# Optimization experiments

Hardware: AMD Instinct MI355X
Metric: run time of the kernel (lower is better)

## Reference

```python
import jax, jax.numpy as jnp
import numpy as np

EPS = 1e-5  # torch BatchNorm2d default eps


def setup_inputs() -> dict:
    key = jax.random.key(0)
    ks = jax.random.split(key, 11)
    n, c, h, w = 16, 512, 64, 64
    grp, cg, mip = 4, 128, 16
    return {
        "x": jax.random.normal(ks[0], (n, c, h, w), dtype=jnp.float32),
        "W1": jax.random.normal(ks[1], (mip, cg), dtype=jnp.float32) * 0.05,
        "b1": jax.random.normal(ks[2], (mip,), dtype=jnp.float32) * 0.05,
        "gamma": jax.random.uniform(ks[3], (mip,), dtype=jnp.float32, minval=0.5, maxval=1.5),
        "beta": jax.random.normal(ks[4], (mip,), dtype=jnp.float32) * 0.05,
        "mean": jax.random.normal(ks[5], (mip,), dtype=jnp.float32) * 0.05,
        "var": jax.random.uniform(ks[6], (mip,), dtype=jnp.float32, minval=0.5, maxval=1.5),
        "Wh": jax.random.normal(ks[7], (cg, mip), dtype=jnp.float32) * 0.1,
        "bh": jax.random.normal(ks[8], (cg,), dtype=jnp.float32) * 0.05,
        "Ww": jax.random.normal(ks[9], (cg, mip), dtype=jnp.float32) * 0.1,
        "bw": jax.random.normal(ks[10], (cg,), dtype=jnp.float32) * 0.05,
    }


def reference(x, W1, b1, gamma, beta, mean, var, Wh, bh, Ww, bw):
    n, c, h, w = x.shape
    grp = 4
    cg = c // grp
    # Since c % 4 == 0, torch.split gives 4 equal groups: fold group into a new axis.
    xg = x.reshape(n, grp, cg, h, w)                       # (n,g,cg,h,w)
    gh = xg.mean(axis=4)                                   # pool over w -> (n,g,cg,h)
    gw = xg.mean(axis=3)                                   # pool over h -> (n,g,cg,w)
    y = jnp.concatenate([gh, gw], axis=3)                  # (n,g,cg,h+w)
    # conv1 (1x1) shared across all 4 groups
    y = jnp.einsum('ngcl,mc->ngml', y, W1) + b1[None, None, :, None]
    # BatchNorm2d (eval mode, running stats)
    scale = gamma / jnp.sqrt(var + EPS)
    y = y * scale[None, None, :, None] + (beta - mean * scale)[None, None, :, None]
    # h_swish: x * relu6(x+3)/6
    y = y * (jnp.clip(y + 3.0, 0.0, 6.0) / 6.0)
    yh, yw = y[..., :h], y[..., h:]                        # (n,g,mip,h), (n,g,mip,w)
    a_h = jax.nn.sigmoid(jnp.einsum('ngml,cm->ngcl', yh, Wh) + bh[None, None, :, None])
    a_w = jax.nn.sigmoid(jnp.einsum('ngml,cm->ngcl', yw, Ww) + bw[None, None, :, None])
    out = xg * a_h[..., :, None] * a_w[..., None, :]       # (n,g,cg,h,w)
    out = out.reshape(n, c, h, w)
    # channel shuffle: (n, cg, grp, h, w) -> permute group axis forward
    out = out.reshape(n, cg, grp, h, w).transpose(0, 2, 1, 3, 4).reshape(n, c, h, w)
    return out
```

## Files before the change

kernel.cpp:

```cpp
#include <hip/hip_runtime.h>

#define N_   16
#define C_   512
#define GRP  4
#define CG   128
#define MIP  16

__device__ __forceinline__ float bf_lo(unsigned u) { return __uint_as_float(u << 16); }
__device__ __forceinline__ float bf_hi(unsigned u) { return __uint_as_float(u & 0xFFFF0000u); }
__device__ __forceinline__ float bf1(unsigned short s) { return __uint_as_float((unsigned)s << 16); }

__device__ __forceinline__ float ld_scalar(const void* p, int i, bool isbf) {
    return isbf ? bf1(((const unsigned short*)p)[i]) : ((const float*)p)[i];
}

__device__ __forceinline__ bool sniff_isbf(const unsigned* __restrict__ x32,
                                           int t, unsigned* s_flag) {
    if (t < 64) {
        int cnt = 0;
        #pragma unroll
        for (int k = 0; k < 4; ++k) {
            unsigned w = x32[t + 64 * k];
            unsigned e = (w >> 7) & 0xFFu;
            cnt += (e >= 0x60u && e <= 0x9Fu) ? 1 : 0;
        }
        #pragma unroll
        for (int off = 32; off > 0; off >>= 1) cnt += __shfl_down(cnt, off, 64);
        if (t == 0) *s_flag = (cnt >= 192) ? 1u : 0u;
    }
    __syncthreads();
    return *s_flag != 0u;
}

__global__ __launch_bounds__(256) void kreduce(const void* __restrict__ xv,
                                               float* __restrict__ gh,
                                               float* __restrict__ gw) {
    __shared__ float scratch[32][65];
    __shared__ unsigned flag_s;
    const int bid = blockIdx.x;
    const int t = threadIdx.x;
    const bool isbf = sniff_isbf((const unsigned*)xv, t, &flag_s);

    if (isbf) {
        const uint4* src = (const uint4*)((const unsigned short*)xv + (size_t)bid * 4096);
        float cp[8] = {0,0,0,0,0,0,0,0};
        #pragma unroll
        for (int hf = 0; hf < 2; ++hf) {
            int idx = t + hf * 256;
            int r = idx >> 3;
            uint4 v = src[idx];
            unsigned uu[4] = {v.x, v.y, v.z, v.w};
            float rp = 0.f;
            #pragma unroll
            for (int k = 0; k < 4; ++k) {
                float f0 = bf_lo(uu[k]), f1 = bf_hi(uu[k]);
                rp += f0 + f1;
                cp[2*k] += f0; cp[2*k+1] += f1;
            }
            rp += __shfl_xor(rp, 1);
            rp += __shfl_xor(rp, 2);
            rp += __shfl_xor(rp, 4);
            if ((t & 7) == 0) gh[(size_t)bid * 64 + r] = rp * (1.f/64.f);
        }
        #pragma unroll
        for (int k = 0; k < 8; ++k) scratch[t >> 3][(t & 7) * 8 + k] = cp[k];
    } else {
        const float4* src = (const float4*)((const float*)xv + (size_t)bid * 4096);
        float cp[4] = {0,0,0,0};
        #pragma unroll
        for (int it = 0; it < 4; ++it) {
            int idx = t + it * 256;
            int r = idx >> 4;
            float4 v = src[idx];
            float rp = (v.x + v.y) + (v.z + v.w);
            cp[0] += v.x; cp[1] += v.y; cp[2] += v.z; cp[3] += v.w;
            rp += __shfl_xor(rp, 1);
            rp += __shfl_xor(rp, 2);
            rp += __shfl_xor(rp, 4);
            rp += __shfl_xor(rp, 8);
            if ((t & 15) == 0) gh[(size_t)bid * 64 + r] = rp * (1.f/64.f);
        }
        #pragma unroll
        for (int k = 0; k < 4; ++k) scratch[t >> 4][(t & 15) * 4 + k] = cp[k];
    }
    __syncthreads();
    if (t < 64) {
        const int nr = isbf ? 32 : 16;
        float s = 0.f;
        for (int i = 0; i < nr; ++i) s += scratch[i][t];
        gw[(size_t)bid * 64 + t] = s * (1.f/64.f);
    }
}

__global__ __launch_bounds__(256) void kmid(
    const void* __restrict__ xv,
    const float* __restrict__ gh, const float* __restrict__ gw,
    const void* __restrict__ W1, const void* __restrict__ b1,
    const void* __restrict__ gamma, const void* __restrict__ beta,
    const void* __restrict__ mean, const void* __restrict__ var,
    const void* __restrict__ Wh, const void* __restrict__ bh,
    const void* __restrict__ Ww, const void* __restrict__ bw,
    float* __restrict__ aH, float* __restrict__ aW)
{
    __shared__ float W1_s[MIP * CG];
    __shared__ float Whw_s[2][CG * MIP];
    __shared__ float y_s[MIP * 128];
    __shared__ float bhw_s[2][CG];
    __shared__ float scale_s[MIP], shift_s[MIP], b1_s[MIP];
    __shared__ unsigned flag_s;

    const int t = threadIdx.x;
    const int ng = blockIdx.x;
    const bool isbf = sniff_isbf((const unsigned*)xv, t, &flag_s);

    if (isbf) {
        uint4 v = ((const uint4*)W1)[t];
        unsigned uu[4] = {v.x, v.y, v.z, v.w};
        #pragma unroll
        for (int k = 0; k < 4; ++k) {
            W1_s[t*8 + 2*k]   = bf_lo(uu[k]);
            W1_s[t*8 + 2*k+1] = bf_hi(uu[k]);
        }
        uint4 a = ((const uint4*)Wh)[t];
        unsigned ua[4] = {a.x, a.y, a.z, a.w};
        #pragma unroll
        for (int k = 0; k < 4; ++k) {
            Whw_s[0][t*8 + 2*k]   = bf_lo(ua[k]);
            Whw_s[0][t*8 + 2*k+1] = bf_hi(ua[k]);
        }
        uint4 c = ((const uint4*)Ww)[t];
        unsigned uc[4] = {c.x, c.y, c.z, c.w};
        #pragma unroll
        for (int k = 0; k < 4; ++k) {
            Whw_s[1][t*8 + 2*k]   = bf_lo(uc[k]);
            Whw_s[1][t*8 + 2*k+1] = bf_hi(uc[k]);
        }
    } else {
        #pragma unroll
        for (int it = 0; it < 2; ++it) {
            int idx = t + 256 * it;
            float4 v = ((const float4*)W1)[idx];
            W1_s[idx*4] = v.x; W1_s[idx*4+1] = v.y; W1_s[idx*4+2] = v.z; W1_s[idx*4+3] = v.w;
            float4 a = ((const float4*)Wh)[idx];
            Whw_s[0][idx*4] = a.x; Whw_s[0][idx*4+1] = a.y; Whw_s[0][idx*4+2] = a.z; Whw_s[0][idx*4+3] = a.w;
            float4 c = ((const float4*)Ww)[idx];
            Whw_s[1][idx*4] = c.x; Whw_s[1][idx*4+1] = c.y; Whw_s[1][idx*4+2] = c.z; Whw_s[1][idx*4+3] = c.w;
        }
    }
    if (t < CG) bhw_s[0][t] = ld_scalar(bh, t, isbf);
    else        bhw_s[1][t - CG] = ld_scalar(bw, t - CG, isbf);
    if (t < MIP) {
        float sc = ld_scalar(gamma, t, isbf) * rsqrtf(ld_scalar(var, t, isbf) + 1e-5f);
        scale_s[t] = sc;
        shift_s[t] = ld_scalar(beta, t, isbf) - ld_scalar(mean, t, isbf) * sc;
        b1_s[t] = ld_scalar(b1, t, isbf);
    }
    __syncthreads();

    {
        const int l = t & 127;
        const int half = t >> 7;
        const float* gbase = (l < 64) ? (gh + (size_t)ng * 8192 + l)
                                      : (gw + (size_t)ng * 8192 + (l - 64));
        float acc[8] = {0,0,0,0,0,0,0,0};
        for (int cc = 0; cc < CG; ++cc) {
            float v = gbase[(size_t)cc * 64];
            #pragma unroll
            for (int mm = 0; mm < 8; ++mm)
                acc[mm] += W1_s[(half*8 + mm) * CG + cc] * v;
        }
        #pragma unroll
        for (int mm = 0; mm < 8; ++mm) {
            int m = half*8 + mm;
            float yv = acc[mm] + b1_s[m];
            yv = yv * scale_s[m] + shift_s[m];
            float hc = fminf(fmaxf(yv + 3.f, 0.f), 6.f);
            y_s[m * 128 + l] = yv * hc * (1.f/6.f);
        }
    }
    __syncthreads();

    for (int k = 0; k < 64; ++k) {
        int out = t + 256 * k;
        int hf = out >> 13;
        int rem = out & 8191;
        int cc = rem >> 6;
        int i = rem & 63;
        float acc = bhw_s[hf][cc];
        #pragma unroll
        for (int m = 0; m < MIP; ++m)
            acc += Whw_s[hf][cc * MIP + m] * y_s[m * 128 + hf * 64 + i];
        float s = 1.f / (1.f + __expf(-acc));
        float* dst = hf ? aW : aH;
        dst[(size_t)ng * 8192 + cc * 64 + i] = s;
    }
}

__global__ __launch_bounds__(256) void kapply(const void* __restrict__ xv,
                                              const float* __restrict__ aH,
                                              const float* __restrict__ aW,
                                              void* __restrict__ outv) {
    __shared__ float ah_s[64], aw_s[64];
    __shared__ unsigned flag_s;
    const int bid = blockIdx.x;
    const int n = bid >> 9;
    const int o = bid & 511;
    const int p = (o & 127) * 4 + (o >> 7);
    const int g = p >> 7, cc = p & 127;
    const int t = threadIdx.x;
    const bool isbf = sniff_isbf((const unsigned*)xv, t, &flag_s);
    const size_t abase = (size_t)(n * 4 + g) * 8192 + (size_t)cc * 64;

    if (isbf) {
        const uint4* src = (const uint4*)((const unsigned short*)xv + ((size_t)n * 512 + p) * 4096);
        uint4 x0 = src[t];
        uint4 x1 = src[t + 256];
        if (t < 64)       ah_s[t]      = aH[abase + t];
        else if (t < 128) aw_s[t - 64] = aW[abase + (t - 64)];
        __syncthreads();
        uint4* dst = (uint4*)((unsigned short*)outv + (size_t)bid * 4096);
        uint4 xr[2] = {x0, x1};
        #pragma unroll
        for (int hf = 0; hf < 2; ++hf) {
            int idx = t + hf * 256;
            int r = idx >> 3, j0 = (idx & 7) * 8;
            float sah = ah_s[r];
            unsigned uu[4] = {xr[hf].x, xr[hf].y, xr[hf].z, xr[hf].w};
            unsigned res[4];
            #pragma unroll
            for (int k = 0; k < 4; ++k) {
                int j = j0 + 2 * k;
                float f0 = bf_lo(uu[k]) * sah * aw_s[j];
                float f1 = bf_hi(uu[k]) * sah * aw_s[j + 1];
                unsigned u0 = __float_as_uint(f0); u0 += 0x7FFFu + ((u0 >> 16) & 1u);
                unsigned u1 = __float_as_uint(f1); u1 += 0x7FFFu + ((u1 >> 16) & 1u);
                res[k] = (u0 >> 16) | (u1 & 0xFFFF0000u);
            }
            uint4 w2; w2.x = res[0]; w2.y = res[1]; w2.z = res[2]; w2.w = res[3];
            dst[idx] = w2;
        }
    } else {
        const float4* src = (const float4*)((const float*)xv + ((size_t)n * 512 + p) * 4096);
        float4 x0 = src[t];
        float4 x1 = src[t + 256];
        float4 x2 = src[t + 512];
        float4 x3 = src[t + 768];
        if (t < 64)       ah_s[t]      = aH[abase + t];
        else if (t < 128) aw_s[t - 64] = aW[abase + (t - 64)];
        __syncthreads();
        float4* dst = (float4*)((float*)outv + (size_t)bid * 4096);
        float4 xr[4] = {x0, x1, x2, x3};
        #pragma unroll
        for (int it = 0; it < 4; ++it) {
            int idx = t + it * 256;
            int r = idx >> 4, j0 = (idx & 15) * 4;
            float sah = ah_s[r];
            float4 v = xr[it];
            v.x *= sah * aw_s[j0];
            v.y *= sah * aw_s[j0 + 1];
            v.z *= sah * aw_s[j0 + 2];
            v.w *= sah * aw_s[j0 + 3];
            dst[idx] = v;
        }
    }
}

extern "C" void kernel_launch(void* const* d_in, const int* in_sizes, int n_in,
                              void* d_out, int out_size, void* d_ws, size_t ws_size,
                              hipStream_t stream) {
    const void* x     = d_in[0];
    const void* W1    = d_in[1];
    const void* b1    = d_in[2];
    const void* gamma = d_in[3];
    const void* beta  = d_in[4];
    const void* mean  = d_in[5];
    const void* var   = d_in[6];
    const void* Wh    = d_in[7];
    const void* bh    = d_in[8];
    const void* Ww    = d_in[9];
    const void* bw    = d_in[10];

    float* ws = (float*)d_ws;
    float* gh = ws;
    float* gw = gh + 524288;
    float* aH = gw + 524288;
    float* aW = aH + 524288;

    kreduce<<<N_ * C_, 256, 0, stream>>>(x, gh, gw);
    kmid<<<N_ * GRP, 256, 0, stream>>>(x, gh, gw, W1, b1, gamma, beta, mean, var,
                                       Wh, bh, Ww, bw, aH, aW);
    kapply<<<N_ * C_, 256, 0, stream>>>(x, aH, aW, d_out);
}
```

Measured before the change: 291.1 us.

## Map each 64x64 channel tile to one wavefront, removing LDS and block barriers

The reduce and apply kernels now give each wavefront two whole channel tiles instead of one tile per 256-thread block. Column sums and broadcasts of the attention vectors use cross-lane shuffles in place of shared memory and __syncthreads. The grid shrinks from 8192 to 1024 blocks, and the dtype sniff becomes a per-wave shuffle reduction. The aim is to cut block scheduling, barrier and LDS overhead in memory-bound kernels. In exchange, each wave keeps more loads in flight serially and there are fewer blocks available to hide latency.

New measurement: 295.3 us. Within noise of the previous version (+1.5%).

```diff
diff --git a/kernel.cpp b/kernel.cpp
--- a/kernel.cpp
+++ b/kernel.cpp
@@ -14,6 +14,20 @@
     return isbf ? bf1(((const unsigned short*)p)[i]) : ((const float*)p)[i];
 }
 
+__device__ __forceinline__ bool wave_sniff_isbf(const unsigned* __restrict__ x32,
+                                                int lane) {
+    int cnt = 0;
+    #pragma unroll
+    for (int k = 0; k < 4; ++k) {
+        unsigned w = x32[lane + 64 * k];
+        unsigned e = (w >> 7) & 0xFFu;
+        cnt += (e >= 0x60u && e <= 0x9Fu) ? 1 : 0;
+    }
+    #pragma unroll
+    for (int off = 32; off > 0; off >>= 1) cnt += __shfl_xor(cnt, off, 64);
+    return cnt >= 192;
+}
+
 __device__ __forceinline__ bool sniff_isbf(const unsigned* __restrict__ x32,
                                            int t, unsigned* s_flag) {
     if (t < 64) {
@@ -35,60 +49,73 @@
 __global__ __launch_bounds__(256) void kreduce(const void* __restrict__ xv,
                                                float* __restrict__ gh,
                                                float* __restrict__ gw) {
-    __shared__ float scratch[32][65];
-    __shared__ unsigned flag_s;
-    const int bid = blockIdx.x;
-    const int t = threadIdx.x;
-    const bool isbf = sniff_isbf((const unsigned*)xv, t, &flag_s);
-
-    if (isbf) {
-        const uint4* src = (const uint4*)((const unsigned short*)xv + (size_t)bid * 4096);
-        float cp[8] = {0,0,0,0,0,0,0,0};
-        #pragma unroll
-        for (int hf = 0; hf < 2; ++hf) {
-            int idx = t + hf * 256;
-            int r = idx >> 3;
-            uint4 v = src[idx];
-            unsigned uu[4] = {v.x, v.y, v.z, v.w};
-            float rp = 0.f;
+    const int lane = threadIdx.x & 63;
+    const int gwid = blockIdx.x * 4 + (threadIdx.x >> 6);
+    const bool isbf = wave_sniff_isbf((const unsigned*)xv, lane);
+
+    #pragma unroll
+    for (int j = 0; j < 2; ++j) {
+        const int tile = gwid * 2 + j;
+        if (isbf) {
+            const uint4* src = (const uint4*)((const unsigned short*)xv + (size_t)tile * 4096);
+            float cp[8] = {0,0,0,0,0,0,0,0};
+            #pragma unroll
+            for (int i = 0; i < 8; ++i) {
+                uint4 v = src[i * 64 + lane];
+                unsigned uu[4] = {v.x, v.y, v.z, v.w};
+                float rp = 0.f;
+                #pragma unroll
+                for (int k = 0; k < 4; ++k) {
+                    float f0 = bf_lo(uu[k]), f1 = bf_hi(uu[k]);
+                    rp += f0 + f1;
+                    cp[2*k] += f0; cp[2*k+1] += f1;
+                }
+                rp += __shfl_xor(rp, 1, 64);
+                rp += __shfl_xor(rp, 2, 64);
+                rp += __shfl_xor(rp, 4, 64);
+                if ((lane & 7) == 0)
+                    gh[(size_t)tile * 64 + i * 8 + (lane >> 3)] = rp * (1.f/64.f);
+            }
+            #pragma unroll
+            for (int k = 0; k < 8; ++k) {
+                cp[k] += __shfl_xor(cp[k], 8, 64);
+                cp[k] += __shfl_xor(cp[k], 16, 64);
+                cp[k] += __shfl_xor(cp[k], 32, 64);
+            }
+            if (lane < 8) {
+                float4 a = make_float4(cp[0], cp[1], cp[2], cp[3]);
+                float4 b = make_float4(cp[4], cp[5], cp[6], cp[7]);
+                a.x *= (1.f/64.f); a.y *= (1.f/64.f); a.z *= (1.f/64.f); a.w *= (1.f/64.f);
+                b.x *= (1.f/64.f); b.y *= (1.f/64.f); b.z *= (1.f/64.f); b.w *= (1.f/64.f);
+                float4* dst = (float4*)(gw + (size_t)tile * 64 + lane * 8);
+                dst[0] = a; dst[1] = b;
+            }
+        } else {
+            const float4* src = (const float4*)((const float*)xv + (size_t)tile * 4096);
+            float cp[4] = {0,0,0,0};
+            #pragma unroll
+            for (int i = 0; i < 16; ++i) {
+                float4 v = src[i * 64 + lane];
+                float rp = (v.x + v.y) + (v.z + v.w);
+                cp[0] += v.x; cp[1] += v.y; cp[2] += v.z; cp[3] += v.w;
+                rp += __shfl_xor(rp, 1, 64);
+                rp += __shfl_xor(rp, 2, 64);
+                rp += __shfl_xor(rp, 4, 64);
+                rp += __shfl_xor(rp, 8, 64);
+                if ((lane & 15) == 0)
+                    gh[(size_t)tile * 64 + i * 4 + (lane >> 4)] = rp * (1.f/64.f);
+            }
             #pragma unroll
             for (int k = 0; k < 4; ++k) {
-                float f0 = bf_lo(uu[k]), f1 = bf_hi(uu[k]);
-                rp += f0 + f1;
-                cp[2*k] += f0; cp[2*k+1] += f1;
-            }
-            rp += __shfl_xor(rp, 1);
-            rp += __shfl_xor(rp, 2);
-            rp += __shfl_xor(rp, 4);
-            if ((t & 7) == 0) gh[(size_t)bid * 64 + r] = rp * (1.f/64.f);
-        }
-        #pragma unroll
-        for (int k = 0; k < 8; ++k) scratch[t >> 3][(t & 7) * 8 + k] = cp[k];
-    } else {
-        const float4* src = (const float4*)((const float*)xv + (size_t)bid * 4096);
-        float cp[4] = {0,0,0,0};
-        #pragma unroll
-        for (int it = 0; it < 4; ++it) {
-            int idx = t + it * 256;
-            int r = idx >> 4;
-            float4 v = src[idx];
-            float rp = (v.x + v.y) + (v.z + v.w);
-            cp[0] += v.x; cp[1] += v.y; cp[2] += v.z; cp[3] += v.w;
-            rp += __shfl_xor(rp, 1);
-            rp += __shfl_xor(rp, 2);
-            rp += __shfl_xor(rp, 4);
-            rp += __shfl_xor(rp, 8);
-            if ((t & 15) == 0) gh[(size_t)bid * 64 + r] = rp * (1.f/64.f);
-        }
-        #pragma unroll
-        for (int k = 0; k < 4; ++k) scratch[t >> 4][(t & 15) * 4 + k] = cp[k];
-    }
-    __syncthreads();
-    if (t < 64) {
-        const int nr = isbf ? 32 : 16;
-        float s = 0.f;
-        for (int i = 0; i < nr; ++i) s += scratch[i][t];
-        gw[(size_t)bid * 64 + t] = s * (1.f/64.f);
+                cp[k] += __shfl_xor(cp[k], 16, 64);
+                cp[k] += __shfl_xor(cp[k], 32, 64);
+            }
+            if (lane < 16) {
+                float4 a = make_float4(cp[0] * (1.f/64.f), cp[1] * (1.f/64.f),
+                                       cp[2] * (1.f/64.f), cp[3] * (1.f/64.f));
+                *(float4*)(gw + (size_t)tile * 64 + lane * 4) = a;
+            }
+        }
     }
 }
 
@@ -200,67 +227,63 @@
                                               const float* __restrict__ aH,
                                               const float* __restrict__ aW,
                                               void* __restrict__ outv) {
-    __shared__ float ah_s[64], aw_s[64];
-    __shared__ unsigned flag_s;
-    const int bid = blockIdx.x;
-    const int n = bid >> 9;
-    const int o = bid & 511;
-    const int p = (o & 127) * 4 + (o >> 7);
-    const int g = p >> 7, cc = p & 127;
-    const int t = threadIdx.x;
-    const bool isbf = sniff_isbf((const unsigned*)xv, t, &flag_s);
-    const size_t abase = (size_t)(n * 4 + g) * 8192 + (size_t)cc * 64;
-
-    if (isbf) {
-        const uint4* src = (const uint4*)((const unsigned short*)xv + ((size_t)n * 512 + p) * 4096);
-        uint4 x0 = src[t];
-        uint4 x1 = src[t + 256];
-        if (t < 64)       ah_s[t]      = aH[abase + t];
-        else if (t < 128) aw_s[t - 64] = aW[abase + (t - 64)];
-        __syncthreads();
-        uint4* dst = (uint4*)((unsigned short*)outv + (size_t)bid * 4096);
-        uint4 xr[2] = {x0, x1};
-        #pragma unroll
-        for (int hf = 0; hf < 2; ++hf) {
-            int idx = t + hf * 256;
-            int r = idx >> 3, j0 = (idx & 7) * 8;
-            float sah = ah_s[r];
-            unsigned uu[4] = {xr[hf].x, xr[hf].y, xr[hf].z, xr[hf].w};
-            unsigned res[4];
-            #pragma unroll
-            for (int k = 0; k < 4; ++k) {
-                int j = j0 + 2 * k;
-                float f0 = bf_lo(uu[k]) * sah * aw_s[j];
-                float f1 = bf_hi(uu[k]) * sah * aw_s[j + 1];
-                unsigned u0 = __float_as_uint(f0); u0 += 0x7FFFu + ((u0 >> 16) & 1u);
-                unsigned u1 = __float_as_uint(f1); u1 += 0x7FFFu + ((u1 >> 16) & 1u);
-                res[k] = (u0 >> 16) | (u1 & 0xFFFF0000u);
-            }
-            uint4 w2; w2.x = res[0]; w2.y = res[1]; w2.z = res[2]; w2.w = res[3];
-            dst[idx] = w2;
-        }
-    } else {
-        const float4* src = (const float4*)((const float*)xv + ((size_t)n * 512 + p) * 4096);
-        float4 x0 = src[t];
-        float4 x1 = src[t + 256];
-        float4 x2 = src[t + 512];
-        float4 x3 = src[t + 768];
-        if (t < 64)       ah_s[t]      = aH[abase + t];
-        else if (t < 128) aw_s[t - 64] = aW[abase + (t - 64)];
-        __syncthreads();
-        float4* dst = (float4*)((float*)outv + (size_t)bid * 4096);
-        float4 xr[4] = {x0, x1, x2, x3};
-        #pragma unroll
-        for (int it = 0; it < 4; ++it) {
-            int idx = t + it * 256;
-            int r = idx >> 4, j0 = (idx & 15) * 4;
-            float sah = ah_s[r];
-            float4 v = xr[it];
-            v.x *= sah * aw_s[j0];
-            v.y *= sah * aw_s[j0 + 1];
-            v.z *= sah * aw_s[j0 + 2];
-            v.w *= sah * aw_s[j0 + 3];
-            dst[idx] = v;
+    const int lane = threadIdx.x & 63;
+    const int gwid = blockIdx.x * 4 + (threadIdx.x >> 6);
+    const bool isbf = wave_sniff_isbf((const unsigned*)xv, lane);
+
+    #pragma unroll
+    for (int j = 0; j < 2; ++j) {
+        const int bid = gwid * 2 + j;
+        const int n = bid >> 9;
+        const int o = bid & 511;
+        const int p = (o & 127) * 4 + (o >> 7);
+        const int g = p >> 7, cc = p & 127;
+        const size_t abase = (size_t)(n * 4 + g) * 8192 + (size_t)cc * 64;
+
+        const float ah_r = aH[abase + lane];
+        const float aw_r = aW[abase + lane];
+
+        if (isbf) {
+            float awv[8];
+            #pragma unroll
+            for (int k = 0; k < 8; ++k)
+                awv[k] = __shfl(aw_r, (lane & 7) * 8 + k, 64);
+            const uint4* src = (const uint4*)((const unsigned short*)xv + ((size_t)n * 512 + p) * 4096);
+            uint4* dst = (uint4*)((unsigned short*)outv + (size_t)bid * 4096);
+            #pragma unroll
+            for (int i = 0; i < 8; ++i) {
+                float sah = __shfl(ah_r, i * 8 + (lane >> 3), 64);
+                uint4 v = src[i * 64 + lane];
+                unsigned uu[4] = {v.x, v.y, v.z, v.w};
+                unsigned res[4];
+                #pragma unroll
+                for (int k = 0; k < 4; ++k) {
+                    float f0 = bf_lo(uu[k]) * sah * awv[2*k];
+                    float f1 = bf_hi(uu[k]) * sah * awv[2*k+1];
+                    unsigned u0 = __float_as_uint(f0); u0 += 0x7FFFu + ((u0 >> 16) & 1u);
+                    unsigned u1 = __float_as_uint(f1); u1 += 0x7FFFu + ((u1 >> 16) & 1u);
+                    res[k] = (u0 >> 16) | (u1 & 0xFFFF0000u);
+                }
+                uint4 w2; w2.x = res[0]; w2.y = res[1]; w2.z = res[2]; w2.w = res[3];
+                dst[i * 64 + lane] = w2;
+            }
+        } else {
+            float awv[4];
+            #pragma unroll
+            for (int k = 0; k < 4; ++k)
+                awv[k] = __shfl(aw_r, (lane & 15) * 4 + k, 64);
+            const float4* src = (const float4*)((const float*)xv + ((size_t)n * 512 + p) * 4096);
+            float4* dst = (float4*)((float*)outv + (size_t)bid * 4096);
+            #pragma unroll
+            for (int i = 0; i < 16; ++i) {
+                float sah = __shfl(ah_r, i * 4 + (lane >> 4), 64);
+                float4 v = src[i * 64 + lane];
+                v.x *= sah * awv[0];
+                v.y *= sah * awv[1];
+                v.z *= sah * awv[2];
+                v.w *= sah * awv[3];
+                dst[i * 64 + lane] = v;
+            }
         }
     }
 }
@@ -286,8 +309,8 @@
     float* aH = gw + 524288;
     float* aW = aH + 524288;
 
-    kreduce<<<N_ * C_, 256, 0, stream>>>(x, gh, gw);
+    kreduce<<<1024, 256, 0, stream>>>(x, gh, gw);
     kmid<<<N_ * GRP, 256, 0, stream>>>(x, gh, gw, W1, b1, gamma, beta, mean, var,
                                        Wh, bh, Ww, bw, aH, aW);
-    kapply<<<N_ * C_, 256, 0, stream>>>(x, aH, aW, d_out);
-}
+    kapply<<<1024, 256, 0, stream>>>(x, aH, aW, d_out);
+}
```
